# Kernel optimization log

Measured on AMD Instinct MI355X. Metric: run time of the kernel, lower is better.

Reference implementation:

```python
import jax, jax.numpy as jnp
import numpy as np

B, L, D, H, DFF, MODES, ELAYERS = 64, 512, 512, 8, 2048, 32, 2
VOCAB, NUM_APP, KERNEL = 10000, 10000, 25
E = D // H


def setup_inputs() -> dict:
    key = jax.random.key(0)
    ks = jax.random.split(key, 16)
    scale = 1.0 / (D * D)  # FourierBlock weight init scale
    return {
        'x_app': jax.random.randint(ks[0], (B, L), 0, VOCAB),
        'x_time': jax.random.uniform(ks[1], (B, L), dtype=jnp.float32),
        'time_vecs': jax.random.normal(ks[2], (B, L, 24), dtype=jnp.float32),
        'targets': jax.random.randint(ks[3], (B,), 0, NUM_APP),
        'app_emb_w': jax.random.normal(ks[4], (VOCAB, D), dtype=jnp.float32) * 0.02,
        'time_w': jax.random.normal(ks[5], (D,), dtype=jnp.float32) * 0.02,
        'time_b': jnp.zeros((D,), jnp.float32),
        'Wq': jax.random.normal(ks[6], (ELAYERS, D, D), dtype=jnp.float32) * 0.02,
        'bq': jnp.zeros((ELAYERS, D), jnp.float32),
        'Wo': jax.random.normal(ks[7], (ELAYERS, D, D), dtype=jnp.float32) * 0.02,
        'bo': jnp.zeros((ELAYERS, D), jnp.float32),
        'four_wr': jax.random.uniform(ks[8], (ELAYERS, H, E, E, MODES), dtype=jnp.float32) * scale,
        'four_wi': jax.random.uniform(ks[9], (ELAYERS, H, E, E, MODES), dtype=jnp.float32) * scale,
        'conv1_w': jax.random.normal(ks[10], (ELAYERS, DFF, D), dtype=jnp.float32) * 0.02,
        'conv2_w': jax.random.normal(ks[11], (ELAYERS, D, DFF), dtype=jnp.float32) * 0.02,
        'norm_w': jnp.ones((D,), jnp.float32),
        'norm_b': jnp.zeros((D,), jnp.float32),
        'proj_w': jax.random.normal(ks[12], (NUM_APP, D + 24), dtype=jnp.float32) * 0.02,
        'proj_b': jnp.zeros((NUM_APP,), jnp.float32),
    }


def moving_avg(x):
    # edge-replicate pad by (K-1)//2 on each side, then AvgPool1d(K, stride=1)
    pad = (KERNEL - 1) // 2
    xp = jnp.pad(x, ((0, 0), (pad, pad), (0, 0)), mode='edge')  # [B, L+K-1, D]
    cs = jnp.cumsum(xp, axis=1)
    cs = jnp.concatenate([jnp.zeros_like(cs[:, :1]), cs], axis=1)
    return (cs[:, KERNEL:] - cs[:, :-KERNEL]) / KERNEL  # [B, L, D]


def series_decomp(x):
    m = moving_avg(x)
    return x - m, m


def my_layernorm(x, w, b, eps=1e-5):
    mu = jnp.mean(x, axis=-1, keepdims=True)
    var = jnp.mean((x - mu) ** 2, axis=-1, keepdims=True)
    xh = (x - mu) * jax.lax.rsqrt(var + eps) * w + b
    # my_Layernorm: subtract per-sample mean over the sequence dim
    return xh - jnp.mean(xh, axis=1, keepdims=True)


def fourier_block(q, wr, wi):
    # q: [B, L, H, E] -> [B, H, E, L]
    Bq, Lq, Hq, Eq = q.shape
    x = jnp.transpose(q, (0, 2, 3, 1))
    x_ft = jnp.fft.rfft(x, axis=-1)             # [B,H,E,L//2+1] complex64
    xs = x_ft[..., :MODES]                      # low-frequency mode selection
    w = (wr + 1j * wi).astype(xs.dtype)         # [H,E,E,M]
    out_sel = jnp.einsum('bhim,hiom->bhom', xs, w)
    out_ft = jnp.zeros((Bq, Hq, Eq, Lq // 2 + 1), dtype=xs.dtype).at[..., :MODES].set(out_sel)
    return jnp.fft.irfft(out_ft, n=Lq, axis=-1)  # [B,H,E,L]


def encoder_layer(x, Wq, bq, Wo, bo, wr, wi, c1, c2):
    Bx, Lx, Dx = x.shape
    q = (x @ Wq.T + bq).reshape(Bx, Lx, H, E)
    out = fourier_block(q, wr, wi)               # [B,H,E,L]
    # faithful to torch: out.view(B, L, -1) is a raw row-major reinterpret
    out = out.reshape(Bx, Lx, H * E)
    new_x = out @ Wo.T + bo
    x = x + new_x
    x, _ = series_decomp(x)
    y = jax.nn.relu(jnp.einsum('bld,fd->blf', x, c1))   # conv1 (1x1, no bias)
    y = jnp.einsum('blf,df->bld', y, c2)                # conv2 (1x1, no bias)
    res, _ = series_decomp(x + y)
    return res


def reference(x_app, x_time, time_vecs, targets, app_emb_w, time_w, time_b,
              Wq, bq, Wo, bo, four_wr, four_wi, conv1_w, conv2_w,
              norm_w, norm_b, proj_w, proj_b):
    x = app_emb_w[x_app] + x_time[..., None] * time_w + time_b  # [B,L,D]
    for l in range(ELAYERS):
        x = encoder_layer(x, Wq[l], bq[l], Wo[l], bo[l],
                          four_wr[l], four_wi[l], conv1_w[l], conv2_w[l])
    x = my_layernorm(x, norm_w, norm_b)
    last = x[:, -1, :]                                   # [B,D]
    out = jnp.concatenate([last, time_vecs[:, -1, :]], axis=1)  # [B,D+24]
    score = out @ proj_w.T + proj_b                      # [B,NUM_APP]
    return score  # mode='predict' returns score
```

## Files before the change

### kernel.cpp

```cpp
#include <hip/hip_runtime.h>


typedef unsigned short u16;
typedef float f32x4 __attribute__((ext_vector_type(4)));
typedef __bf16 bf16x8 __attribute__((ext_vector_type(8)));

__device__ __forceinline__ u16 f2b(float f) {
  unsigned u = __float_as_uint(f);
  return (u16)((u + 0x7FFFu + ((u >> 16) & 1u)) >> 16);
}
__device__ __forceinline__ float b2f(u16 v) {
  return __uint_as_float((unsigned)v << 16);
}
__device__ __forceinline__ f32x4 b4f(ushort4 v) {
  f32x4 r;
  r.x = b2f(v.x); r.y = b2f(v.y); r.z = b2f(v.z); r.w = b2f(v.w);
  return r;
}

__device__ __forceinline__ void gll16(const void* g, void* l) {
  __builtin_amdgcn_global_load_lds(
      (const __attribute__((address_space(1))) void*)g,
      (__attribute__((address_space(3))) void*)l, 16, 0, 0);
}

template<bool SWAP>
__device__ __forceinline__ f32x4 mfma16(bf16x8 a, bf16x8 b, f32x4 c) {
  if constexpr (SWAP)
    return __builtin_amdgcn_mfma_f32_16x16x32_bf16(b, a, c, 0, 0, 0);
  else
    return __builtin_amdgcn_mfma_f32_16x16x32_bf16(a, b, c, 0, 0, 0);
}

template<bool BIAS, bool RELU, bool RES, bool OUTBF16, bool GUARD, bool TRANS,
         bool SWZ>
__global__ __launch_bounds__(256, 3)
void k_gemm(const u16* __restrict__ A, const u16* __restrict__ B,
            const float* __restrict__ bias, const u16* __restrict__ res,
            float* __restrict__ Cf, u16* __restrict__ Cb,
            int M, int N, int K,
            long zA, long zB, long zC, int nbn, int nbm)
{
  __shared__ __align__(16) u16 sA[2][128 * 32];
  __shared__ __align__(16) u16 sB[2][128 * 32];
  const int tid = threadIdx.x;
  const int wave = tid >> 6, lane = tid & 63;
  int bn, bm;
  if (SWZ) {
    int bid = blockIdx.x;
    int xcd = bid & 7, loc = bid >> 3;
    bn = loc % nbn;
    bm = xcd * (nbm >> 3) + loc / nbn;
  } else {
    bn = blockIdx.x;
    bm = blockIdx.y;
  }
  const int bz = blockIdx.z;
  const int wm = (wave >> 1) * 64, wn = (wave & 1) * 64;

  A += (size_t)bz * zA;
  B += (size_t)bz * zB;

  const int r0 = tid >> 2;
  const int lg = tid & 3;
  const int ps = lg ^ ((r0 >> 1) & 3);
  int gmA0 = bm * 128 + r0, gmA1 = gmA0 + 64;
  int gnB0 = bn * 128 + r0, gnB1 = gnB0 + 64;
  if (GUARD) {
    gmA0 = gmA0 < M ? gmA0 : M - 1;
    gmA1 = gmA1 < M ? gmA1 : M - 1;
    gnB0 = gnB0 < N ? gnB0 : N - 1;
    gnB1 = gnB1 < N ? gnB1 : N - 1;
  }
  const size_t rb = (size_t)K * 2;
  const char* pa0 = (const char*)A + (size_t)gmA0 * rb + lg * 16;
  const char* pa1 = (const char*)A + (size_t)gmA1 * rb + lg * 16;
  const char* pb0 = (const char*)B + (size_t)gnB0 * rb + lg * 16;
  const char* pb1 = (const char*)B + (size_t)gnB1 * rb + lg * 16;
  const int w0 = r0 * 32 + ps * 8;

  f32x4 acc[4][4];
  const f32x4 z = {0.f, 0.f, 0.f, 0.f};
#pragma unroll
  for (int i = 0; i < 4; ++i)
#pragma unroll
    for (int j = 0; j < 4; ++j) acc[i][j] = z;

  const int r = lane & 15, qd = lane >> 4;
  const int pA = (qd ^ ((lane >> 1) & 3)) * 8;
  const int nk = K >> 5;

  uint4 va0, va1, vb0, vb1;
  auto gload = [&](int kt) {
    const size_t ko = (size_t)kt * 64;
    va0 = *(const uint4*)(pa0 + ko);
    va1 = *(const uint4*)(pa1 + ko);
    vb0 = *(const uint4*)(pb0 + ko);
    vb1 = *(const uint4*)(pb1 + ko);
  };

  gload(0);
  int pg = 0;
  for (int kt = 0; kt < nk; ++kt) {
    *(uint4*)&sA[pg][w0]        = va0;
    *(uint4*)&sA[pg][w0 + 2048] = va1;
    *(uint4*)&sB[pg][w0]        = vb0;
    *(uint4*)&sB[pg][w0 + 2048] = vb1;
    if (kt + 1 < nk) gload(kt + 1);
    __syncthreads();
    bf16x8 af[4], bg[4];
#pragma unroll
    for (int mi = 0; mi < 4; ++mi)
      af[mi] = *(const bf16x8*)&sA[pg][(wm + mi * 16 + r) * 32 + pA];
#pragma unroll
    for (int ni = 0; ni < 4; ++ni)
      bg[ni] = *(const bf16x8*)&sB[pg][(wn + ni * 16 + r) * 32 + pA];
#pragma unroll
    for (int mi = 0; mi < 4; ++mi)
#pragma unroll
      for (int ni = 0; ni < 4; ++ni)
        acc[mi][ni] = mfma16<!TRANS>(af[mi], bg[ni], acc[mi][ni]);
    pg ^= 1;
  }

  if (Cf) Cf += (size_t)bz * zC;
  if (Cb) Cb += (size_t)bz * zC;

  if constexpr (!TRANS) {
#pragma unroll
    for (int mi = 0; mi < 4; ++mi) {
      const int gm = bm * 128 + wm + mi * 16 + r;
      if (GUARD && gm >= M) continue;
#pragma unroll
      for (int ni = 0; ni < 4; ++ni) {
        const int gn0 = bn * 128 + wn + ni * 16 + qd * 4;
        if (GUARD && gn0 >= N) continue;
        float v[4];
        ushort4 rv;
        if (RES) rv = *(const ushort4*)&res[(size_t)gm * N + gn0];
#pragma unroll
        for (int e = 0; e < 4; ++e) {
          v[e] = acc[mi][ni][e];
          if (BIAS) v[e] += bias[gn0 + e];
          if (RES)  v[e] += b2f(e == 0 ? rv.x : e == 1 ? rv.y : e == 2 ? rv.z : rv.w);
          if (RELU) v[e] = v[e] > 0.f ? v[e] : 0.f;
        }
        if (OUTBF16) {
          ushort4 o;
          o.x = f2b(v[0]); o.y = f2b(v[1]); o.z = f2b(v[2]); o.w = f2b(v[3]);
          *(ushort4*)&Cb[(size_t)gm * N + gn0] = o;
        } else {
          float4 o = {v[0], v[1], v[2], v[3]};
          *(float4*)&Cf[(size_t)gm * N + gn0] = o;
        }
      }
    }
  } else {
#pragma unroll
    for (int ni = 0; ni < 4; ++ni) {
      const int gn = bn * 128 + wn + ni * 16 + r;
      if (GUARD && gn >= N) continue;
      const float bb = BIAS ? bias[gn] : 0.f;
#pragma unroll
      for (int mi = 0; mi < 4; ++mi) {
        const int gm0 = bm * 128 + wm + mi * 16 + qd * 4;
        if (GUARD && gm0 >= M) continue;
        float v[4];
#pragma unroll
        for (int e = 0; e < 4; ++e) {
          v[e] = acc[mi][ni][e];
          if (BIAS) v[e] += bb;
          if (RELU) v[e] = v[e] > 0.f ? v[e] : 0.f;
        }
        if (OUTBF16) {
          ushort4 o;
          o.x = f2b(v[0]); o.y = f2b(v[1]); o.z = f2b(v[2]); o.w = f2b(v[3]);
          *(ushort4*)&Cb[(size_t)gn * M + gm0] = o;
        } else {
          float4 o = {v[0], v[1], v[2], v[3]};
          *(float4*)&Cf[(size_t)gn * M + gm0] = o;
        }
      }
    }
  }
}

template<bool BIAS, bool RELU, bool RES, bool TRANS>
__global__ __launch_bounds__(512, 2)
void k_gemm3(const u16* __restrict__ A, const u16* __restrict__ B,
             const float* __restrict__ bias, const u16* __restrict__ res,
             u16* __restrict__ C, int M, int N, int K,
             int nbn, int nbm, long zA, long zC)
{
  __shared__ __align__(16) u16 sA[2][2][256 * 32];
  __shared__ __align__(16) u16 sB[2][2][256 * 32];
  const int tid = threadIdx.x;
  const int w8 = tid >> 6, lane = tid & 63;
  const int bid = blockIdx.x;
  const int xcd = bid & 7, loc = bid >> 3;
  const int mpx = (int)(gridDim.x >> 3) / nbn;
  const int mflat = xcd * mpx + loc / nbn;
  const int bn = loc % nbn;
  const int bz = mflat / nbm;
  const int bm = mflat - bz * nbm;
  const int wm = (w8 >> 2) * 128, wn = (w8 & 3) * 64;

  A += (size_t)bz * zA;

  const int r0 = tid >> 2;
  const int lg = (tid & 3) ^ ((r0 >> 1) & 3);
  const u16* pA0 = A + (size_t)(bm * 256 + r0) * K + lg * 8;
  const u16* pA1 = pA0 + (size_t)128 * K;
  const u16* pB0 = B + (size_t)(bn * 256 + r0) * K + lg * 8;
  const u16* pB1 = pB0 + (size_t)128 * K;
  const int la0 = w8 * 512;
  const int la1 = 4096 + w8 * 512;

  const int nk = K >> 6;

  auto stA = [&](int t, int ks) {
    const size_t ko = (size_t)(t << 6) + (size_t)(ks << 5);
    u16* d = &sA[t & 1][ks][0];
    gll16(pA0 + ko, d + la0);
    gll16(pA1 + ko, d + la1);
  };
  auto stB = [&](int t, int ks) {
    const size_t ko = (size_t)(t << 6) + (size_t)(ks << 5);
    u16* d = &sB[t & 1][ks][0];
    gll16(pB0 + ko, d + la0);
    gll16(pB1 + ko, d + la1);
  };

  f32x4 acc[8][4];
  const f32x4 z = {0.f, 0.f, 0.f, 0.f};
#pragma unroll
  for (int i = 0; i < 8; ++i)
#pragma unroll
    for (int j = 0; j < 4; ++j) acc[i][j] = z;

  const int fr = lane & 15, qd = lane >> 4;
  const int pAo = ((qd ^ ((lane >> 1) & 3)) << 3);

  stA(0, 0); stB(0, 0); stA(0, 1); stB(0, 1);
  asm volatile("s_waitcnt vmcnt(4)" ::: "memory");
  __builtin_amdgcn_s_barrier();
  asm volatile("" ::: "memory");

  for (int t = 0; t < nk; ++t) {
    const int c = t & 1;
    bf16x8 af[4], bgk[4];
#pragma unroll
    for (int i = 0; i < 4; ++i)
      af[i] = *(const bf16x8*)&sA[c][0][(wm + i * 16 + fr) * 32 + pAo];
#pragma unroll
    for (int i = 0; i < 4; ++i)
      bgk[i] = *(const bf16x8*)&sB[c][0][(wn + i * 16 + fr) * 32 + pAo];
    if (t + 1 < nk) stA(t + 1, 0);
    __builtin_amdgcn_s_setprio(1);
#pragma unroll
    for (int mi = 0; mi < 4; ++mi)
#pragma unroll
      for (int ni = 0; ni < 4; ++ni)
        acc[mi][ni] = __builtin_amdgcn_mfma_f32_16x16x32_bf16(
            af[mi], bgk[ni], acc[mi][ni], 0, 0, 0);
    __builtin_amdgcn_s_setprio(0);
#pragma unroll
    for (int i = 0; i < 4; ++i)
      af[i] = *(const bf16x8*)&sA[c][0][(wm + 64 + i * 16 + fr) * 32 + pAo];
    if (t + 1 < nk) stB(t + 1, 0);
    if (t == nk - 1) asm volatile("s_waitcnt vmcnt(0)" ::: "memory");
    else             asm volatile("s_waitcnt vmcnt(4)" ::: "memory");
    __builtin_amdgcn_s_barrier();
    asm volatile("" ::: "memory");
    __builtin_amdgcn_s_setprio(1);
#pragma unroll
    for (int mi = 0; mi < 4; ++mi)
#pragma unroll
      for (int ni = 0; ni < 4; ++ni)
        acc[4 + mi][ni] = __builtin_amdgcn_mfma_f32_16x16x32_bf16(
            af[mi], bgk[ni], acc[4 + mi][ni], 0, 0, 0);
    __builtin_amdgcn_s_setprio(0);
#pragma unroll
    for (int i = 0; i < 4; ++i)
      af[i] = *(const bf16x8*)&sA[c][1][(wm + i * 16 + fr) * 32 + pAo];
#pragma unroll
    for (int i = 0; i < 4; ++i)
      bgk[i] = *(const bf16x8*)&sB[c][1][(wn + i * 16 + fr) * 32 + pAo];
    if (t + 1 < nk) stA(t + 1, 1);
    __builtin_amdgcn_s_setprio(1);
#pragma unroll
    for (int mi = 0; mi < 4; ++mi)
#pragma unroll
      for (int ni = 0; ni < 4; ++ni)
        acc[mi][ni] = __builtin_amdgcn_mfma_f32_16x16x32_bf16(
            af[mi], bgk[ni], acc[mi][ni], 0, 0, 0);
    __builtin_amdgcn_s_setprio(0);
#pragma unroll
    for (int i = 0; i < 4; ++i)
      af[i] = *(const bf16x8*)&sA[c][1][(wm + 64 + i * 16 + fr) * 32 + pAo];
    if (t + 1 < nk) stB(t + 1, 1);
    if (t + 1 < nk) asm volatile("s_waitcnt vmcnt(4)" ::: "memory");
    __builtin_amdgcn_s_barrier();
    asm volatile("" ::: "memory");
    __builtin_amdgcn_s_setprio(1);
#pragma unroll
    for (int mi = 0; mi < 4; ++mi)
#pragma unroll
      for (int ni = 0; ni < 4; ++ni)
        acc[4 + mi][ni] = __builtin_amdgcn_mfma_f32_16x16x32_bf16(
            af[mi], bgk[ni], acc[4 + mi][ni], 0, 0, 0);
    __builtin_amdgcn_s_setprio(0);
  }

  C += (size_t)bz * zC;
#pragma unroll
  for (int mi = 0; mi < 8; ++mi) {
#pragma unroll
    for (int ni = 0; ni < 4; ++ni) {
#pragma unroll
      for (int e = 0; e < 4; ++e) {
        int gm = bm * 256 + wm + mi * 16 + qd * 4 + e;
        int gn = bn * 256 + wn + ni * 16 + fr;
        float v = acc[mi][ni][e];
        if (BIAS) v += bias[gn];
        if (RES)  v += b2f(res[(size_t)gm * N + gn]);
        if (RELU) v = v > 0.f ? v : 0.f;
        size_t oi = TRANS ? ((size_t)gn * M + gm) : ((size_t)gm * N + gn);
        C[oi] = f2b(v);
      }
    }
  }
}

__global__ void k_basis(u16* __restrict__ dftB, u16* __restrict__ Binv)
{
  int id = blockIdx.x * 256 + threadIdx.x;
  if (id >= 32768) return;
  {
    int m = id >> 9, l = id & 511;
    int mm = m & 31;
    float ang = (float)((l * mm) & 511) * (6.283185307179586f / 512.f);
    float s, c;
    __sincosf(ang, &s, &c);
    dftB[id] = f2b(m < 32 ? c : -s);
  }
  {
    int l = id >> 6, m = id & 63;
    int mm = m & 31;
    float ang = (float)((l * mm) & 511) * (6.283185307179586f / 512.f);
    float s, c;
    __sincosf(ang, &s, &c);
    float v;
    if (m < 32) v = (m == 0 ? 1.f : 2.f) * (1.f / 512.f) * c;
    else        v = (mm == 0 ? 0.f : (-2.f / 512.f) * s);
    Binv[id] = f2b(v);
  }
}

__global__ void k_wb(const float* __restrict__ wo, const u16* __restrict__ Binv,
                     u16* __restrict__ wb)
{
  __shared__ float part[4][64];
  int blk = blockIdx.x;
  int t = threadIdx.x;
  int m = t & 63, q = t >> 6;
  const float* wrow = wo + (size_t)blk * 512;
  float a = 0.f;
#pragma unroll 4
  for (int l = q * 128; l < q * 128 + 128; ++l)
    a += wrow[l] * b2f(Binv[l * 64 + m]);
  part[q][m] = a;
  __syncthreads();
  if (t < 64) {
    float v = part[0][t] + part[1][t] + part[2][t] + part[3][t];
    wb[(size_t)blk * 64 + t] = f2b(v);
  }
}

__global__ void k_convert3(const float* __restrict__ wq, u16* __restrict__ wqo,
                           const float* __restrict__ c1, u16* __restrict__ c1o,
                           const float* __restrict__ c2, u16* __restrict__ c2o)
{
  int id = blockIdx.x * 256 + threadIdx.x;
  if (id < 524288)       wqo[id]           = f2b(wq[id]);
  else if (id < 2621440) c1o[id - 524288]  = f2b(c1[id - 524288]);
  else                   c2o[id - 2621440] = f2b(c2[id - 2621440]);
}

__global__ void k_convproj(const float* __restrict__ w, u16* __restrict__ o)
{
  int id = blockIdx.x * 256 + threadIdx.x;
  if (id >= 10000 * 544) return;
  int n = id / 544, k = id % 544;
  o[id] = f2b(k < 536 ? w[(size_t)n * 536 + k] : 0.f);
}

__global__ void k_transp(const float* __restrict__ wr, const float* __restrict__ wi,
                         float* __restrict__ wrT, float* __restrict__ wiT)
{
  __shared__ float tr[64 * 33], ti[64 * 33];
  int blk = blockIdx.x;
  int t = threadIdx.x;
  int lh = blk >> 6, i = blk & 63;
  const size_t src = (size_t)blk * 2048;
#pragma unroll
  for (int p = 0; p < 8; ++p) {
    int id = p * 256 + t;
    int o = id >> 5, m = id & 31;
    tr[o * 33 + m] = wr[src + id];
    ti[o * 33 + m] = wi[src + id];
  }
  __syncthreads();
#pragma unroll
  for (int p = 0; p < 8; ++p) {
    int id = p * 256 + t;
    int m = id >> 6, o = id & 63;
    size_t dst = ((size_t)(lh * 32 + m) * 64 + i) * 64 + o;
    wrT[dst] = tr[o * 33 + m];
    wiT[dst] = ti[o * 33 + m];
  }
}

__global__ void k_embed(const int* __restrict__ xapp, const float* __restrict__ xtime,
                        const float* __restrict__ emb, const float* __restrict__ tw,
                        const float* __restrict__ tb, u16* __restrict__ xb)
{
  int id = blockIdx.x * 256 + threadIdx.x;
  int j = id & 127, bl = id >> 7;
  float4 e = ((const float4*)emb)[(size_t)xapp[bl] * 128 + j];
  float t = xtime[bl];
  float4 w4 = ((const float4*)tw)[j];
  float4 b4 = ((const float4*)tb)[j];
  ushort4 o;
  o.x = f2b(e.x + t * w4.x + b4.x);
  o.y = f2b(e.y + t * w4.y + b4.y);
  o.z = f2b(e.z + t * w4.z + b4.z);
  o.w = f2b(e.w + t * w4.w + b4.w);
  ((ushort4*)xb)[id] = o;
}

__global__ __launch_bounds__(256)
void k_mix(const float* __restrict__ spec, const float* __restrict__ wrT,
           const float* __restrict__ wiT, u16* __restrict__ Ab)
{
  __shared__ float swr[4096], swi[4096];
  __shared__ float sre[4][64], sim[4][64];
  int hm = blockIdx.x;
  int bg = blockIdx.y;
  int h = hm >> 5, m = hm & 31, t = threadIdx.x;
  const float* wrb = wrT + (size_t)hm * 4096;
  const float* wib = wiT + (size_t)hm * 4096;
#pragma unroll
  for (int p = 0; p < 16; ++p) {
    int id = p * 256 + t;
    swr[id] = wrb[id];
    swi[id] = wib[id];
  }
  int o = t & 63, bsub = t >> 6;
  for (int b0 = 0; b0 < 16; b0 += 4) {
    __syncthreads();
    int b = bg * 16 + b0 + bsub;
    const float* spb = spec + (size_t)b * 32768;
    sre[bsub][o] = spb[m * 512 + h * 64 + o];
    sim[bsub][o] = spb[(32 + m) * 512 + h * 64 + o];
    __syncthreads();
    float aR = 0.f, aI = 0.f;
#pragma unroll 8
    for (int i = 0; i < 64; ++i) {
      float xr = sre[bsub][i], xi = sim[bsub][i];
      float wrv = swr[i * 64 + o], wiv = swi[i * 64 + o];
      aR += xr * wrv - xi * wiv;
      aI += xr * wiv + xi * wrv;
    }
    size_t row = (size_t)b * 512 + h * 64 + o;
    Ab[row * 64 + m] = f2b(aR);
    Ab[row * 64 + 32 + m] = f2b(aI);
  }
}

__global__ void k_decomp(const u16* __restrict__ in, u16* __restrict__ outb)
{
  int blk = blockIdx.x;
  int j = blk >> 3;
  int b = (blk & 7) + 8 * (j >> 3);
  int ck = (j & 7) * 2 + (threadIdx.x >> 7);
  int d4 = threadIdx.x & 127;
  const ushort4* xb = (const ushort4*)(in + (size_t)b * 262144) + d4;
  ushort4* ob = (ushort4*)(outb + (size_t)b * 262144) + d4;
  int l0 = ck * 32;
  f32x4 sum = {0.f, 0.f, 0.f, 0.f};
#pragma unroll
  for (int jj = -12; jj <= 12; ++jj) {
    int idx = l0 + jj;
    idx = idx < 0 ? 0 : idx;
    sum += b4f(xb[idx * 128]);
  }
#pragma unroll 4
  for (int l = l0; l < l0 + 32; ++l) {
    f32x4 xv = b4f(xb[l * 128]);
    f32x4 o = xv - sum * (1.f / 25.f);
    ushort4 ov;
    ov.x = f2b(o.x); ov.y = f2b(o.y); ov.z = f2b(o.z); ov.w = f2b(o.w);
    ob[l * 128] = ov;
    int ia = l + 13 > 511 ? 511 : l + 13;
    int ir = l - 12 < 0 ? 0 : l - 12;
    sum += b4f(xb[ia * 128]) - b4f(xb[ir * 128]);
  }
}

__global__ void k_lnstats(const u16* __restrict__ x, float* __restrict__ mu,
                          float* __restrict__ rs)
{
  int row = blockIdx.x;
  const u16* xr = x + (size_t)row * 512;
  int t = threadIdx.x;
  ushort2 p = ((const ushort2*)xr)[t];
  float v0 = b2f(p.x), v1 = b2f(p.y);
  float s = v0 + v1, ss = v0 * v0 + v1 * v1;
#pragma unroll
  for (int off = 32; off; off >>= 1) {
    s += __shfl_down(s, off);
    ss += __shfl_down(ss, off);
  }
  __shared__ float as[4], ass[4];
  if ((t & 63) == 0) { as[t >> 6] = s; ass[t >> 6] = ss; }
  __syncthreads();
  if (t == 0) {
    float S = as[0] + as[1] + as[2] + as[3];
    float SS = ass[0] + ass[1] + ass[2] + ass[3];
    float m = S * (1.f / 512.f);
    float var = SS * (1.f / 512.f) - m * m;
    mu[row] = m;
    rs[row] = rsqrtf(var + 1e-5f);
  }
}

__global__ void k_lastcat1(const u16* __restrict__ x, const float* __restrict__ mu,
                           const float* __restrict__ rs, float* __restrict__ part)
{
  int b = blockIdx.x >> 3, g = blockIdx.x & 7, t = threadIdx.x;
  const u16* xb = x + (size_t)b * 262144;
  const float* mub = mu + b * 512;
  const float* rsb = rs + b * 512;
  float a0 = 0.f, a1 = 0.f;
#pragma unroll 4
  for (int l = g * 64; l < g * 64 + 64; ++l) {
    float m = mub[l], rr = rsb[l];
    ushort2 p = ((const ushort2*)(xb + l * 512))[t];
    a0 += (b2f(p.x) - m) * rr;
    a1 += (b2f(p.y) - m) * rr;
  }
  part[((size_t)b * 8 + g) * 512 + 2 * t]     = a0;
  part[((size_t)b * 8 + g) * 512 + 2 * t + 1] = a1;
}

__global__ void k_lastcat2(const u16* __restrict__ x, const float* __restrict__ mu,
                           const float* __restrict__ rs, const float* __restrict__ part,
                           const float* __restrict__ nw, u16* __restrict__ cat)
{
  int b = blockIdx.x, t = threadIdx.x;
#pragma unroll
  for (int hh = 0; hh < 2; ++hh) {
    int d = t + hh * 256;
    float acc = 0.f;
#pragma unroll
    for (int g = 0; g < 8; ++g)
      acc += part[((size_t)b * 8 + g) * 512 + d];
    float lastv = (b2f(x[(size_t)b * 262144 + 511 * 512 + d]) - mu[b * 512 + 511])
                  * rs[b * 512 + 511];
    cat[b * 544 + d] = f2b(nw[d] * (lastv - acc * (1.f / 512.f)));
  }
}

__global__ void k_timecat(const float* __restrict__ tv, u16* __restrict__ cat)
{
  int id = blockIdx.x * 256 + threadIdx.x;
  if (id >= 2048) return;
  int b = id >> 5, j = id & 31;
  int pos = 512 + j;
  float v = (pos < 536) ? tv[((size_t)b * 512 + 511) * 24 + (pos - 512)] : 0.f;
  cat[b * 544 + pos] = f2b(v);
}

extern "C" void kernel_launch(void* const* d_in, const int* in_sizes, int n_in,
                              void* d_out, int out_size, void* d_ws, size_t ws_size,
                              hipStream_t stream)
{
  (void)in_sizes; (void)n_in; (void)out_size; (void)ws_size;
  const int*   x_app  = (const int*)  d_in[0];
  const float* x_time = (const float*)d_in[1];
  const float* tvec   = (const float*)d_in[2];
  const float* emb    = (const float*)d_in[4];
  const float* time_w = (const float*)d_in[5];
  const float* time_b = (const float*)d_in[6];
  const float* Wq     = (const float*)d_in[7];
  const float* bq     = (const float*)d_in[8];
  const float* Wo     = (const float*)d_in[9];
  const float* bo     = (const float*)d_in[10];
  const float* fwr    = (const float*)d_in[11];
  const float* fwi    = (const float*)d_in[12];
  const float* c1     = (const float*)d_in[13];
  const float* c2     = (const float*)d_in[14];
  const float* norm_w = (const float*)d_in[15];
  const float* proj_w = (const float*)d_in[17];
  const float* proj_b = (const float*)d_in[18];
  float* out = (float*)d_out;

  char* w = (char*)d_ws;
  auto alloc = [&](size_t bytes) -> char* {
    char* p = w;
    w += (bytes + 255) & ~(size_t)255;
    return p;
  };
  u16*   Cb   = (u16*)  alloc(33554432);
  u16*   YqT  = (u16*)  alloc(134217728);
  u16*   T1b  = (u16*)  alloc(33554432);
  float* S1   = (float*)alloc(8388608);
  u16*   Coef = (u16*)  alloc(4194304);
  float* wrT  = (float*)alloc(2 * 1048576 * 4);
  float* wiT  = (float*)alloc(2 * 1048576 * 4);
  u16*   wqb  = (u16*)  alloc(2 * 262144 * 2);
  u16*   wbb  = (u16*)  alloc(2 * 512 * 64 * 2);
  u16*   c1b  = (u16*)  alloc(2 * 1048576 * 2);
  u16*   c2b  = (u16*)  alloc(2 * 1048576 * 2);
  u16*   pwb  = (u16*)  alloc(10000 * 544 * 2);
  u16*   dftB = (u16*)  alloc(64 * 512 * 2);
  u16*   Binv = (u16*)  alloc(512 * 64 * 2);
  float* muB  = (float*)alloc(131072);
  float* rsB  = (float*)alloc(131072);
  float* part = (float*)alloc(64 * 8 * 512 * 4);
  u16*   cat  = (u16*)  alloc(64 * 544 * 2);

  k_basis<<<128, 256, 0, stream>>>(dftB, Binv);
  k_wb<<<1024, 256, 0, stream>>>(Wo, Binv, wbb);
  k_transp<<<1024, 256, 0, stream>>>(fwr, fwi, wrT, wiT);
  k_convert3<<<18432, 256, 0, stream>>>(Wq, wqb, c1, c1b, c2, c2b);
  k_convproj<<<21250, 256, 0, stream>>>(proj_w, pwb);
  k_embed<<<16384, 256, 0, stream>>>(x_app, x_time, emb, time_w, time_b, Cb);

  for (int l = 0; l < 2; ++l) {
    const u16* wq_l = wqb + l * 262144;
    const u16* wb_l = wbb + l * 32768;
    const u16* c1_l = c1b + l * 1048576;
    const u16* c2_l = c2b + l * 1048576;

    k_gemm3<true, false, false, true>
        <<<256, 512, 0, stream>>>(
        Cb, wq_l, bq + l * 512, nullptr, YqT, 512, 512, 512,
        2, 2, 262144, 262144);
    k_gemm<false, false, false, false, true, true, false>
        <<<dim3(1, 4, 64), 256, 0, stream>>>(
        YqT, dftB, nullptr, nullptr, S1, nullptr, 512, 64, 512,
        262144, 0, 32768, 0, 0);
    k_mix<<<dim3(256, 4), 256, 0, stream>>>(
        S1, wrT + l * 1048576, wiT + l * 1048576, Coef);
    k_gemm<true, false, true, true, false, false, true>
        <<<dim3(1024, 1, 1), 256, 0, stream>>>(
        Coef, wb_l, bo + l * 512, Cb, nullptr, T1b, 32768, 512, 64,
        0, 0, 0, 4, 256);
    k_decomp<<<512, 256, 0, stream>>>(T1b, Cb);
    k_gemm3<false, true, false, false>
        <<<1024, 512, 0, stream>>>(
        Cb, c1_l, nullptr, nullptr, YqT, 32768, 2048, 512,
        8, 128, 0, 0);
    k_gemm3<false, false, true, false>
        <<<256, 512, 0, stream>>>(
        YqT, c2_l, nullptr, Cb, T1b, 32768, 512, 2048,
        2, 128, 0, 0);
    k_decomp<<<512, 256, 0, stream>>>(T1b, Cb);
  }

  k_lnstats<<<32768, 256, 0, stream>>>(Cb, muB, rsB);
  k_lastcat1<<<512, 256, 0, stream>>>(Cb, muB, rsB, part);
  k_lastcat2<<<64, 256, 0, stream>>>(Cb, muB, rsB, part, norm_w, cat);
  k_timecat<<<8, 256, 0, stream>>>(tvec, cat);
  k_gemm<true, false, false, false, true, false, false>
      <<<dim3(79, 1, 1), 256, 0, stream>>>(
      cat, pwb, proj_b, nullptr, out, nullptr, 64, 10000, 544,
      0, 0, 0, 0, 0);
}
```

Before: 776.9 us.

## Switch big GEMMs to 4-wave blocks with 128x128 per-wave tiles

The 256x256 block GEMM now runs with 4 waves of 256 threads instead of 8 waves, and each wave computes a 128x128 sub-tile (8x8 MFMA accumulators) instead of 128x64. Each thread issues 4 global-to-LDS loads per stage instead of 2, and the k-loop drops from four barrier phases per iteration to two. The goal is more register-level reuse of A/B fragments per LDS read and fewer barriers. In exchange, each wave holds 256 accumulator registers, which lowers occupancy (launch bounds 256,1) and gives less latency hiding, with possible register spills.

Result: slower. 896.9 us (+15.4%).

```diff
diff --git a/kernel.cpp b/kernel.cpp
--- a/kernel.cpp
+++ b/kernel.cpp
@@ -186,8 +186,8 @@
 }
 
 template<bool BIAS, bool RELU, bool RES, bool TRANS>
-__global__ __launch_bounds__(512, 2)
-void k_gemm3(const u16* __restrict__ A, const u16* __restrict__ B,
+__global__ __launch_bounds__(256, 1)
+void k_gemm4(const u16* __restrict__ A, const u16* __restrict__ B,
              const float* __restrict__ bias, const u16* __restrict__ res,
              u16* __restrict__ C, int M, int N, int K,
              int nbn, int nbm, long zA, long zC)
@@ -195,7 +195,7 @@
   __shared__ __align__(16) u16 sA[2][2][256 * 32];
   __shared__ __align__(16) u16 sB[2][2][256 * 32];
   const int tid = threadIdx.x;
-  const int w8 = tid >> 6, lane = tid & 63;
+  const int w4 = tid >> 6, lane = tid & 63;
   const int bid = blockIdx.x;
   const int xcd = bid & 7, loc = bid >> 3;
   const int mpx = (int)(gridDim.x >> 3) / nbn;
@@ -203,120 +203,95 @@
   const int bn = loc % nbn;
   const int bz = mflat / nbm;
   const int bm = mflat - bz * nbm;
-  const int wm = (w8 >> 2) * 128, wn = (w8 & 3) * 64;
+  const int wm = (w4 >> 1) * 128, wn = (w4 & 1) * 128;
 
   A += (size_t)bz * zA;
 
   const int r0 = tid >> 2;
   const int lg = (tid & 3) ^ ((r0 >> 1) & 3);
   const u16* pA0 = A + (size_t)(bm * 256 + r0) * K + lg * 8;
-  const u16* pA1 = pA0 + (size_t)128 * K;
   const u16* pB0 = B + (size_t)(bn * 256 + r0) * K + lg * 8;
-  const u16* pB1 = pB0 + (size_t)128 * K;
-  const int la0 = w8 * 512;
-  const int la1 = 4096 + w8 * 512;
+  const int la = w4 * 512;
 
   const int nk = K >> 6;
 
   auto stA = [&](int t, int ks) {
     const size_t ko = (size_t)(t << 6) + (size_t)(ks << 5);
-    u16* d = &sA[t & 1][ks][0];
-    gll16(pA0 + ko, d + la0);
-    gll16(pA1 + ko, d + la1);
+    u16* d = &sA[t & 1][ks][0] + la;
+#pragma unroll
+    for (int j = 0; j < 4; ++j)
+      gll16(pA0 + (size_t)(j * 64) * K + ko, d + j * 2048);
   };
   auto stB = [&](int t, int ks) {
     const size_t ko = (size_t)(t << 6) + (size_t)(ks << 5);
-    u16* d = &sB[t & 1][ks][0];
-    gll16(pB0 + ko, d + la0);
-    gll16(pB1 + ko, d + la1);
+    u16* d = &sB[t & 1][ks][0] + la;
+#pragma unroll
+    for (int j = 0; j < 4; ++j)
+      gll16(pB0 + (size_t)(j * 64) * K + ko, d + j * 2048);
   };
 
-  f32x4 acc[8][4];
+  f32x4 acc[8][8];
   const f32x4 z = {0.f, 0.f, 0.f, 0.f};
 #pragma unroll
   for (int i = 0; i < 8; ++i)
 #pragma unroll
-    for (int j = 0; j < 4; ++j) acc[i][j] = z;
+    for (int j = 0; j < 8; ++j) acc[i][j] = z;
 
   const int fr = lane & 15, qd = lane >> 4;
   const int pAo = ((qd ^ ((lane >> 1) & 3)) << 3);
 
   stA(0, 0); stB(0, 0); stA(0, 1); stB(0, 1);
-  asm volatile("s_waitcnt vmcnt(4)" ::: "memory");
+  asm volatile("s_waitcnt vmcnt(8)" ::: "memory");
   __builtin_amdgcn_s_barrier();
   asm volatile("" ::: "memory");
 
   for (int t = 0; t < nk; ++t) {
     const int c = t & 1;
-    bf16x8 af[4], bgk[4];
-#pragma unroll
-    for (int i = 0; i < 4; ++i)
+    bf16x8 af[8], bgk[8];
+#pragma unroll
+    for (int i = 0; i < 8; ++i)
       af[i] = *(const bf16x8*)&sA[c][0][(wm + i * 16 + fr) * 32 + pAo];
 #pragma unroll
-    for (int i = 0; i < 4; ++i)
+    for (int i = 0; i < 8; ++i)
       bgk[i] = *(const bf16x8*)&sB[c][0][(wn + i * 16 + fr) * 32 + pAo];
-    if (t + 1 < nk) stA(t + 1, 0);
+    if (t + 1 < nk) { stA(t + 1, 0); stB(t + 1, 0); }
+    if (t == nk - 1) asm volatile("s_waitcnt vmcnt(0)" ::: "memory");
+    else             asm volatile("s_waitcnt vmcnt(8)" ::: "memory");
+    __builtin_amdgcn_s_barrier();
+    asm volatile("" ::: "memory");
     __builtin_amdgcn_s_setprio(1);
 #pragma unroll
-    for (int mi = 0; mi < 4; ++mi)
-#pragma unroll
-      for (int ni = 0; ni < 4; ++ni)
+    for (int mi = 0; mi < 8; ++mi)
+#pragma unroll
+      for (int ni = 0; ni < 8; ++ni)
         acc[mi][ni] = __builtin_amdgcn_mfma_f32_16x16x32_bf16(
             af[mi], bgk[ni], acc[mi][ni], 0, 0, 0);
     __builtin_amdgcn_s_setprio(0);
 #pragma unroll
-    for (int i = 0; i < 4; ++i)
-      af[i] = *(const bf16x8*)&sA[c][0][(wm + 64 + i * 16 + fr) * 32 + pAo];
-    if (t + 1 < nk) stB(t + 1, 0);
-    if (t == nk - 1) asm volatile("s_waitcnt vmcnt(0)" ::: "memory");
-    else             asm volatile("s_waitcnt vmcnt(4)" ::: "memory");
+    for (int i = 0; i < 8; ++i)
+      af[i] = *(const bf16x8*)&sA[c][1][(wm + i * 16 + fr) * 32 + pAo];
+#pragma unroll
+    for (int i = 0; i < 8; ++i)
+      bgk[i] = *(const bf16x8*)&sB[c][1][(wn + i * 16 + fr) * 32 + pAo];
+    if (t + 1 < nk) { stA(t + 1, 1); stB(t + 1, 1); }
+    if (t + 1 < nk) asm volatile("s_waitcnt vmcnt(8)" ::: "memory");
     __builtin_amdgcn_s_barrier();
     asm volatile("" ::: "memory");
     __builtin_amdgcn_s_setprio(1);
 #pragma unroll
-    for (int mi = 0; mi < 4; ++mi)
-#pragma unroll
-      for (int ni = 0; ni < 4; ++ni)
-        acc[4 + mi][ni] = __builtin_amdgcn_mfma_f32_16x16x32_bf16(
-            af[mi], bgk[ni], acc[4 + mi][ni], 0, 0, 0);
-    __builtin_amdgcn_s_setprio(0);
-#pragma unroll
-    for (int i = 0; i < 4; ++i)
-      af[i] = *(const bf16x8*)&sA[c][1][(wm + i * 16 + fr) * 32 + pAo];
-#pragma unroll
-    for (int i = 0; i < 4; ++i)
-      bgk[i] = *(const bf16x8*)&sB[c][1][(wn + i * 16 + fr) * 32 + pAo];
-    if (t + 1 < nk) stA(t + 1, 1);
-    __builtin_amdgcn_s_setprio(1);
-#pragma unroll
-    for (int mi = 0; mi < 4; ++mi)
-#pragma unroll
-      for (int ni = 0; ni < 4; ++ni)
+    for (int mi = 0; mi < 8; ++mi)
+#pragma unroll
+      for (int ni = 0; ni < 8; ++ni)
         acc[mi][ni] = __builtin_amdgcn_mfma_f32_16x16x32_bf16(
             af[mi], bgk[ni], acc[mi][ni], 0, 0, 0);
     __builtin_amdgcn_s_setprio(0);
-#pragma unroll
-    for (int i = 0; i < 4; ++i)
-      af[i] = *(const bf16x8*)&sA[c][1][(wm + 64 + i * 16 + fr) * 32 + pAo];
-    if (t + 1 < nk) stB(t + 1, 1);
-    if (t + 1 < nk) asm volatile("s_waitcnt vmcnt(4)" ::: "memory");
-    __builtin_amdgcn_s_barrier();
-    asm volatile("" ::: "memory");
-    __builtin_amdgcn_s_setprio(1);
-#pragma unroll
-    for (int mi = 0; mi < 4; ++mi)
-#pragma unroll
-      for (int ni = 0; ni < 4; ++ni)
-        acc[4 + mi][ni] = __builtin_amdgcn_mfma_f32_16x16x32_bf16(
-            af[mi], bgk[ni], acc[4 + mi][ni], 0, 0, 0);
-    __builtin_amdgcn_s_setprio(0);
   }
 
   C += (size_t)bz * zC;
 #pragma unroll
   for (int mi = 0; mi < 8; ++mi) {
 #pragma unroll
-    for (int ni = 0; ni < 4; ++ni) {
+    for (int ni = 0; ni < 8; ++ni) {
 #pragma unroll
       for (int e = 0; e < 4; ++e) {
         int gm = bm * 256 + wm + mi * 16 + qd * 4 + e;
@@ -644,8 +619,8 @@
     const u16* c1_l = c1b + l * 1048576;
     const u16* c2_l = c2b + l * 1048576;
 
-    k_gemm3<true, false, false, true>
-        <<<256, 512, 0, stream>>>(
+    k_gemm4<true, false, false, true>
+        <<<256, 256, 0, stream>>>(
         Cb, wq_l, bq + l * 512, nullptr, YqT, 512, 512, 512,
         2, 2, 262144, 262144);
     k_gemm<false, false, false, false, true, true, false>
@@ -659,12 +634,12 @@
         Coef, wb_l, bo + l * 512, Cb, nullptr, T1b, 32768, 512, 64,
         0, 0, 0, 4, 256);
     k_decomp<<<512, 256, 0, stream>>>(T1b, Cb);
-    k_gemm3<false, true, false, false>
-        <<<1024, 512, 0, stream>>>(
+    k_gemm4<false, true, false, false>
+        <<<1024, 256, 0, stream>>>(
         Cb, c1_l, nullptr, nullptr, YqT, 32768, 2048, 512,
         8, 128, 0, 0);
-    k_gemm3<false, false, true, false>
-        <<<256, 512, 0, stream>>>(
+    k_gemm4<false, false, true, false>
+        <<<256, 256, 0, stream>>>(
         YqT, c2_l, nullptr, Cb, T1b, 32768, 512, 2048,
         2, 128, 0, 0);
     k_decomp<<<512, 256, 0, stream>>>(T1b, Cb);
```
